# Performance work log

Hardware: AMD Instinct MI355X
Metric: run time of the kernel (lower is better)

The kernel has to match this reference:

```python
import jax, jax.numpy as jnp
import numpy as np
from jax import lax

K = 3
PAD = 1
STRIDE = 1


def setup_inputs() -> dict:
    key = jax.random.key(0)
    k1, k2, k3 = jax.random.split(key, 3)
    B, Cin, Cout, H, W = 4, 64, 64, 128, 128
    x = jax.random.normal(k1, (B, Cin, H, W), dtype=jnp.float32)
    # offset-generating conv weight: [2*K*K, Cin, K, K]
    w_offset = jax.random.normal(k2, (2 * K * K, Cin, K, K), dtype=jnp.float32) * 0.05
    # deformable conv weight: [Cout, Cin, K, K]
    w_deform = jax.random.normal(k3, (Cout, Cin, K, K), dtype=jnp.float32) * 0.05
    return {"x": x, "w_offset": w_offset, "w_deform": w_deform}


def _bilinear_sample_one(img, ys, xs):
    # img: [C, H, W]; ys, xs: [K2, Ho, Wo] float sampling coords
    H, W = img.shape[1], img.shape[2]
    y0 = jnp.floor(ys)
    x0 = jnp.floor(xs)
    wy = ys - y0  # frac weights, [K2, Ho, Wo]
    wx = xs - x0

    def gather(yi, xi):
        valid = (yi >= 0) & (yi <= H - 1) & (xi >= 0) & (xi <= W - 1)
        yc = jnp.clip(yi, 0, H - 1).astype(jnp.int32)
        xc = jnp.clip(xi, 0, W - 1).astype(jnp.int32)
        # img[:, yc, xc] -> [C, K2, Ho, Wo]; zero outside (torchvision zero-pad)
        return img[:, yc, xc] * valid[None].astype(img.dtype)

    v00 = gather(y0, x0)
    v01 = gather(y0, x0 + 1)
    v10 = gather(y0 + 1, x0)
    v11 = gather(y0 + 1, x0 + 1)
    w00 = ((1 - wy) * (1 - wx))[None]
    w01 = ((1 - wy) * wx)[None]
    w10 = (wy * (1 - wx))[None]
    w11 = (wy * wx)[None]
    return v00 * w00 + v01 * w01 + v10 * w10 + v11 * w11  # [C, K2, Ho, Wo]


def reference(x, w_offset, w_deform):
    B, Cin, H, W = x.shape
    Cout = w_deform.shape[0]
    K2 = K * K
    # 1) plain conv to produce offsets: [B, 2*K2, H, W]
    offset = lax.conv_general_dilated(
        x, w_offset, window_strides=(STRIDE, STRIDE),
        padding=((PAD, PAD), (PAD, PAD)),
        dimension_numbers=("NCHW", "OIHW", "NCHW"))
    Ho, Wo = offset.shape[2], offset.shape[3]
    # torchvision ordering: channel 2*k = dy, 2*k+1 = dx, taps row-major
    off = offset.reshape(B, K2, 2, Ho, Wo)
    dy, dx = off[:, :, 0], off[:, :, 1]  # [B, K2, Ho, Wo]
    # 2) base sampling grid per kernel tap
    kk = jnp.arange(K2)
    ki = (kk // K).astype(jnp.float32)  # tap row
    kj = (kk % K).astype(jnp.float32)   # tap col
    base_y = (jnp.arange(Ho, dtype=jnp.float32) * STRIDE - PAD)[None, :] + ki[:, None]  # [K2, Ho]
    base_x = (jnp.arange(Wo, dtype=jnp.float32) * STRIDE - PAD)[None, :] + kj[:, None]  # [K2, Wo]
    ys = base_y[None, :, :, None] + dy  # [B, K2, Ho, Wo]
    xs = base_x[None, :, None, :] + dx
    # 3) deformable bilinear gather: [B, Cin, K2, Ho, Wo]
    sampled = jax.vmap(_bilinear_sample_one)(x, ys, xs)
    # 4) weighted accumulation (the conv contraction)
    out = jnp.einsum("ock,bckhw->bohw", w_deform.reshape(Cout, Cin, K2), sampled)
    return out
```

## Files before the change

### kernel.cpp

```cpp
#include <hip/hip_runtime.h>


#define BATCH 4
#define CIN   64
#define COUT  64
#define HH    128
#define WW    128
#define HWPIX (HH*WW)

typedef __attribute__((ext_vector_type(8))) short short8;
typedef __attribute__((ext_vector_type(4))) float floatx4;
typedef __attribute__((ext_vector_type(2))) float f32x2;

__device__ __forceinline__ unsigned short f2bf(float f) {
  unsigned int u = __float_as_uint(f);
  unsigned int r = u + 0x7fffu + ((u >> 16) & 1u);
  return (unsigned short)(r >> 16);
}
__device__ __forceinline__ float bf2f(unsigned short h) { return __uint_as_float(((unsigned int)h) << 16); }
__device__ __forceinline__ float lo16f(unsigned int u) { return __uint_as_float(u << 16); }
__device__ __forceinline__ float hi16f(unsigned int u) { return __uint_as_float(u & 0xffff0000u); }

__device__ __forceinline__ unsigned int bilin2v(unsigned int u00, unsigned int u01,
                                                unsigned int u10, unsigned int u11,
                                                f32x2 w00, f32x2 w01, f32x2 w10, f32x2 w11) {
  f32x2 c00 = {lo16f(u00), hi16f(u00)};
  f32x2 c01 = {lo16f(u01), hi16f(u01)};
  f32x2 c10 = {lo16f(u10), hi16f(u10)};
  f32x2 c11 = {lo16f(u11), hi16f(u11)};
  f32x2 a = c00 * w00 + c01 * w01 + c10 * w10 + c11 * w11;
  unsigned int r;
  asm("v_cvt_pk_bf16_f32 %0, %1, %2" : "=v"(r) : "v"(a.x), "v"(a.y));
  return r;
}

__device__ __forceinline__ int swz(int a) { return a ^ (((a >> 9) & 3) << 4); }

__global__ __launch_bounds__(256) void pre_kernel(const float* __restrict__ x,
                                                  const float* __restrict__ wo,
                                                  const float* __restrict__ wd,
                                                  unsigned short* __restrict__ xThi,
                                                  unsigned short* __restrict__ xTlo,
                                                  unsigned short* __restrict__ wdA,
                                                  unsigned short* __restrict__ woAhi,
                                                  unsigned short* __restrict__ woAlo) {
  int tid = threadIdx.x;
  if (blockIdx.x < 4096) {
    __shared__ float tile[32][33];
    int t = blockIdx.x;
    int b = t >> 10, rem = t & 1023;
    int c0 = (rem >> 9) * 32, p0 = (rem & 511) * 32;
    int tx = tid & 31, ty = tid >> 5;
    const float* xb = x + (size_t)b * CIN * HWPIX;
    size_t boff = (size_t)b * HWPIX * CIN;
#pragma unroll
    for (int i = 0; i < 4; i++)
      tile[ty + i * 8][tx] = xb[(size_t)(c0 + ty + i * 8) * HWPIX + p0 + tx];
    __syncthreads();
#pragma unroll
    for (int i = 0; i < 2; i++) {
      int tt = tid + i * 256;
      int row = tt >> 4;
      int cp = tt & 15;
      float v0 = tile[cp * 2][row], v1 = tile[cp * 2 + 1][row];
      unsigned short h0 = f2bf(v0), h1 = f2bf(v1);
      unsigned short l0 = f2bf(v0 - bf2f(h0)), l1 = f2bf(v1 - bf2f(h1));
      size_t o = boff + (size_t)(p0 + row) * CIN + c0 + cp * 2;
      *(ushort2*)&xThi[o] = make_ushort2(h0, h1);
      *(ushort2*)&xTlo[o] = make_ushort2(l0, l1);
    }
  } else {
    int t = (blockIdx.x - 4096) * 256 + tid;
    if (t < 36864) {
      int j = t & 7, lane = (t >> 3) & 63, ct = (t >> 9) & 3, kc = (t >> 11) & 1, kk = t >> 12;
      int cout = ct * 16 + (lane & 15);
      int cin  = kc * 32 + (lane >> 4) * 8 + j;
      wdA[t] = f2bf(wd[(size_t)(cout * CIN + cin) * 9 + kk]);
    }
    int t2 = t - 36864;
    if (t2 >= 0 && t2 < 18432) {
      int j = t2 & 7, lane = (t2 >> 3) & 63, ct = (t2 >> 9) & 1, kc = (t2 >> 10) & 1, kk = t2 >> 11;
      int cout = ct * 16 + (lane & 15);
      int cin  = kc * 32 + (lane >> 4) * 8 + j;
      float v = (cout < 18) ? wo[(size_t)(cout * CIN + cin) * 9 + kk] : 0.f;
      unsigned short h = f2bf(v);
      woAhi[t2] = h;
      woAlo[t2] = f2bf(v - bf2f(h));
    }
  }
}

__global__ __launch_bounds__(256, 4) void fused_dcn_kernel(const unsigned short* __restrict__ xThi,
                                                           const unsigned short* __restrict__ xTlo,
                                                           const unsigned short* __restrict__ woAhi,
                                                           const unsigned short* __restrict__ woAlo,
                                                           const unsigned short* __restrict__ wdA,
                                                           float* __restrict__ out) {
  __shared__ unsigned short sBhi2[2][4096];
  __shared__ unsigned short sBlo2[2][4096];
  __shared__ float offL[18 * 64];
  char* sHc = (char*)sBhi2;
  char* sLc = (char*)sBlo2;

  int tid = threadIdx.x;
  int hw = blockIdx.x;
  int bid = (hw & 7) * 128 + (hw >> 3);
  int b = bid >> 8, r = bid & 255, y = r >> 1, x0 = (r & 1) << 6;

  int p1 = tid >> 2, si = tid & 3;
  int lane = tid & 63, w = tid >> 6;

  const unsigned short* xhib = xThi + (size_t)b * HWPIX * CIN;
  const unsigned short* xlob = xTlo + (size_t)b * HWPIX * CIN;

  int wq = p1 >> 4, iq = p1 & 15;
  int kcd = si >> 1, qb = si & 1;
  int wb0 = ((((wq * 2 + kcd) * 64) + qb * 32 + iq) * 8) * 2;
  int wb1 = wb0 + 256;
  int swb0 = swz(wb0), swb1 = swz(wb1);
  int brb0[4], brb1[4];
#pragma unroll
  for (int pg = 0; pg < 4; pg++) {
    brb0[pg] = swz(pg * 2048 + lane * 16);
    brb1[pg] = swz(pg * 2048 + 1024 + lane * 16);
  }

  int xp = x0 + p1;

  floatx4 oacc[2];
  oacc[0] = (floatx4){0.f, 0.f, 0.f, 0.f};
  oacc[1] = (floatx4){0.f, 0.f, 0.f, 0.f};
  int ctA = w & 1, pgA = (w >> 1) * 2;

  auto ldA = [&](int kk, uint4& h0, uint4& h1, uint4& l0, uint4& l1) {
    int ys = y - 1 + kk / 3;
    int xs = xp - 1 + kk % 3;
    bool valid = (ys >= 0) && (ys < HH) && (xs >= 0) && (xs < WW);
    h0 = (uint4){0, 0, 0, 0}; h1 = h0; l0 = h0; l1 = h0;
    if (valid) {
      const unsigned short* ph = xhib + (size_t)(ys * WW + xs) * CIN + si * 16;
      const unsigned short* pl = xlob + (size_t)(ys * WW + xs) * CIN + si * 16;
      h0 = *(const uint4*)ph; h1 = *(const uint4*)(ph + 8);
      l0 = *(const uint4*)pl; l1 = *(const uint4*)(pl + 8);
    }
  };
  auto stageA = [&](int nxt, const uint4& h0, const uint4& h1, const uint4& l0, const uint4& l1) {
    *(uint4*)(sHc + nxt * 8192 + swb0) = h0;
    *(uint4*)(sHc + nxt * 8192 + swb1) = h1;
    *(uint4*)(sLc + nxt * 8192 + swb0) = l0;
    *(uint4*)(sLc + nxt * 8192 + swb1) = l1;
  };
  auto mfmaA = [&](int kk, int cur) {
    const short8* Ah = (const short8*)(woAhi + (size_t)kk * 2048);
    const short8* Al = (const short8*)(woAlo + (size_t)kk * 2048);
    short8 ah0 = Ah[ctA * 64 + lane], ah1 = Ah[128 + ctA * 64 + lane];
    short8 al0 = Al[ctA * 64 + lane], al1 = Al[128 + ctA * 64 + lane];
#pragma unroll
    for (int pgi = 0; pgi < 2; pgi++) {
      int pg = pgA + pgi;
      short8 bh0 = *(const short8*)(sHc + cur * 8192 + brb0[pg]);
      short8 bh1 = *(const short8*)(sHc + cur * 8192 + brb1[pg]);
      short8 bl0 = *(const short8*)(sLc + cur * 8192 + brb0[pg]);
      short8 bl1 = *(const short8*)(sLc + cur * 8192 + brb1[pg]);
      oacc[pgi] = __builtin_amdgcn_mfma_f32_16x16x32_bf16(ah0, bh0, oacc[pgi], 0, 0, 0);
      oacc[pgi] = __builtin_amdgcn_mfma_f32_16x16x32_bf16(ah0, bl0, oacc[pgi], 0, 0, 0);
      oacc[pgi] = __builtin_amdgcn_mfma_f32_16x16x32_bf16(al0, bh0, oacc[pgi], 0, 0, 0);
      oacc[pgi] = __builtin_amdgcn_mfma_f32_16x16x32_bf16(ah1, bh1, oacc[pgi], 0, 0, 0);
      oacc[pgi] = __builtin_amdgcn_mfma_f32_16x16x32_bf16(ah1, bl1, oacc[pgi], 0, 0, 0);
      oacc[pgi] = __builtin_amdgcn_mfma_f32_16x16x32_bf16(al1, bh1, oacc[pgi], 0, 0, 0);
    }
  };

  {
    uint4 h0s[2], h1s[2], l0s[2], l1s[2];
    ldA(0, h0s[0], h1s[0], l0s[0], l1s[0]);
    stageA(0, h0s[0], h1s[0], l0s[0], l1s[0]);
    ldA(1, h0s[1], h1s[1], l0s[1], l1s[1]);
    __syncthreads();
#pragma unroll
    for (int kk = 0; kk < 9; kk++) {
      if (kk < 7) ldA(kk + 2, h0s[kk & 1], h1s[kk & 1], l0s[kk & 1], l1s[kk & 1]);
      __builtin_amdgcn_sched_barrier(0);
      if (kk < 8) stageA((kk + 1) & 1, h0s[(kk + 1) & 1], h1s[(kk + 1) & 1],
                         l0s[(kk + 1) & 1], l1s[(kk + 1) & 1]);
      mfmaA(kk, kk & 1);
      __syncthreads();
    }
  }

  {
    int rowb = (lane >> 4) * 4;
    int colb = pgA * 16 + (lane & 15);
#pragma unroll
    for (int pgi = 0; pgi < 2; pgi++)
#pragma unroll
      for (int rr = 0; rr < 4; rr++) {
        int row = ctA * 16 + rowb + rr;
        if (row < 18) offL[row * 64 + colb + pgi * 16] = oacc[pgi][rr];
      }
  }
  __syncthreads();

  floatx4 acc[4];
#pragma unroll
  for (int pg = 0; pg < 4; pg++) acc[pg] = (floatx4){0.f, 0.f, 0.f, 0.f};

  struct BS {
    float w00, w01, w10, w11;
    uint4 a00, a01, a10, a11, b00, b01, b10, b11;
  };
  auto ldB = [&](int kk) -> BS {
    BS s;
    float dy = offL[(2 * kk) * 64 + p1];
    float dx = offL[(2 * kk + 1) * 64 + p1];
    float ys = (float)(y - 1 + kk / 3) + dy;
    float xs = (float)(xp - 1 + kk % 3) + dx;
    float y0f = floorf(ys), x0f = floorf(xs);
    float wy = ys - y0f, wx = xs - x0f;
    int iy0 = (int)y0f, ix0 = (int)x0f;
    int iy1 = iy0 + 1, ix1 = ix0 + 1;
    s.w00 = (1.f - wy) * (1.f - wx); s.w01 = (1.f - wy) * wx;
    s.w10 = wy * (1.f - wx);         s.w11 = wy * wx;
    bool vy0 = (iy0 >= 0) && (iy0 < HH), vy1 = (iy1 >= 0) && (iy1 < HH);
    bool vx0 = (ix0 >= 0) && (ix0 < WW), vx1 = (ix1 >= 0) && (ix1 < WW);
    if (!(vy0 && vx0)) s.w00 = 0.f;
    if (!(vy0 && vx1)) s.w01 = 0.f;
    if (!(vy1 && vx0)) s.w10 = 0.f;
    if (!(vy1 && vx1)) s.w11 = 0.f;
    int cy0 = min(max(iy0, 0), HH - 1), cy1 = min(max(iy1, 0), HH - 1);
    int cx0 = min(max(ix0, 0), WW - 1), cx1 = min(max(ix1, 0), WW - 1);
    const unsigned short* q00 = xhib + (size_t)(cy0 * WW + cx0) * CIN + si * 16;
    const unsigned short* q01 = xhib + (size_t)(cy0 * WW + cx1) * CIN + si * 16;
    const unsigned short* q10 = xhib + (size_t)(cy1 * WW + cx0) * CIN + si * 16;
    const unsigned short* q11 = xhib + (size_t)(cy1 * WW + cx1) * CIN + si * 16;
    s.a00 = *(const uint4*)q00; s.a01 = *(const uint4*)q01;
    s.a10 = *(const uint4*)q10; s.a11 = *(const uint4*)q11;
    s.b00 = *(const uint4*)(q00 + 8); s.b01 = *(const uint4*)(q01 + 8);
    s.b10 = *(const uint4*)(q10 + 8); s.b11 = *(const uint4*)(q11 + 8);
    return s;
  };
  auto blendStoreB = [&](int nxt, const BS& s) {
    f32x2 w00 = {s.w00, s.w00}, w01 = {s.w01, s.w01};
    f32x2 w10 = {s.w10, s.w10}, w11 = {s.w11, s.w11};
    uint4 o0, o1;
    o0.x = bilin2v(s.a00.x, s.a01.x, s.a10.x, s.a11.x, w00, w01, w10, w11);
    o0.y = bilin2v(s.a00.y, s.a01.y, s.a10.y, s.a11.y, w00, w01, w10, w11);
    o0.z = bilin2v(s.a00.z, s.a01.z, s.a10.z, s.a11.z, w00, w01, w10, w11);
    o0.w = bilin2v(s.a00.w, s.a01.w, s.a10.w, s.a11.w, w00, w01, w10, w11);
    o1.x = bilin2v(s.b00.x, s.b01.x, s.b10.x, s.b11.x, w00, w01, w10, w11);
    o1.y = bilin2v(s.b00.y, s.b01.y, s.b10.y, s.b11.y, w00, w01, w10, w11);
    o1.z = bilin2v(s.b00.z, s.b01.z, s.b10.z, s.b11.z, w00, w01, w10, w11);
    o1.w = bilin2v(s.b00.w, s.b01.w, s.b10.w, s.b11.w, w00, w01, w10, w11);
    *(uint4*)(sHc + nxt * 8192 + swb0) = o0;
    *(uint4*)(sHc + nxt * 8192 + swb1) = o1;
  };
  auto mfmaB = [&](int kk, int cur) {
    const short8* Ap = (const short8*)(wdA + (size_t)kk * 4096);
    short8 a0 = Ap[w * 64 + lane];
    short8 a1 = Ap[256 + w * 64 + lane];
#pragma unroll
    for (int pg = 0; pg < 4; pg++) {
      short8 bv0 = *(const short8*)(sHc + cur * 8192 + brb0[pg]);
      short8 bv1 = *(const short8*)(sHc + cur * 8192 + brb1[pg]);
      acc[pg] = __builtin_amdgcn_mfma_f32_16x16x32_bf16(a0, bv0, acc[pg], 0, 0, 0);
      acc[pg] = __builtin_amdgcn_mfma_f32_16x16x32_bf16(a1, bv1, acc[pg], 0, 0, 0);
    }
  };

  {
    BS sb[2];
    sb[0] = ldB(0);
    blendStoreB(0, sb[0]);
    sb[1] = ldB(1);
    __syncthreads();
#pragma unroll
    for (int kk = 0; kk < 9; kk++) {
      if (kk < 7) sb[kk & 1] = ldB(kk + 2);
      __builtin_amdgcn_sched_barrier(0);
      if (kk < 8) blendStoreB((kk + 1) & 1, sb[(kk + 1) & 1]);
      mfmaB(kk, kk & 1);
      __syncthreads();
    }
  }

  int rowb = (lane >> 4) * 4;
  float* outb = out + (size_t)b * COUT * HWPIX + y * WW + x0 + (lane & 15);
#pragma unroll
  for (int pg = 0; pg < 4; pg++)
#pragma unroll
    for (int rr = 0; rr < 4; rr++)
      outb[(size_t)(w * 16 + rowb + rr) * HWPIX + pg * 16] = acc[pg][rr];
}

extern "C" void kernel_launch(void* const* d_in, const int* in_sizes, int n_in,
                              void* d_out, int out_size, void* d_ws, size_t ws_size,
                              hipStream_t stream) {
  const float* x  = (const float*)d_in[0];
  const float* wo = (const float*)d_in[1];
  const float* wd = (const float*)d_in[2];
  float* out = (float*)d_out;

  char* wsb = (char*)d_ws;
  unsigned short* xThi  = (unsigned short*)wsb;
  unsigned short* xTlo  = (unsigned short*)(wsb + 8388608);
  unsigned short* wdA   = (unsigned short*)(wsb + 16777216);
  unsigned short* woAhi = (unsigned short*)(wsb + 16777216 + 73728);
  unsigned short* woAlo = (unsigned short*)(wsb + 16850944 + 36864);

  pre_kernel<<<dim3(4096 + 216), dim3(256), 0, stream>>>(x, wo, wd, xThi, xTlo, wdA, woAhi, woAlo);
  fused_dcn_kernel<<<dim3(BATCH * HWPIX / 64), dim3(256), 0, stream>>>(xThi, xTlo, woAhi, woAlo, wdA, out);
}
```

Before: 104.9 us.

## Pad transposed input with zero halo and stream offset-conv tiles via global_load_lds

The preprocessing kernel now writes the bf16 hi/lo channel-last input into a 130x130 zero-padded buffer and zeroes the halo with extra blocks. The offset-conv stage drops per-thread bounds checks and register staging, and loads tiles straight into LDS with async global_load_lds using a new XOR swizzle for the MFMA B reads. The aim is to cut register pressure, VALU address work and the register-to-LDS copy in the first GEMM. The cost is a simpler single-stage prefetch pipeline and a slightly larger workspace.

```diff
diff --git a/kernel.cpp b/kernel.cpp
--- a/kernel.cpp
+++ b/kernel.cpp
@@ -7,6 +7,9 @@
 #define HH    128
 #define WW    128
 #define HWPIX (HH*WW)
+#define PADW  130
+#define PADROW (PADW*64)
+#define PADIMG (PADW*PADW*64)
 
 typedef __attribute__((ext_vector_type(8))) short short8;
 typedef __attribute__((ext_vector_type(4))) float floatx4;
@@ -36,11 +39,14 @@
 
 __device__ __forceinline__ int swz(int a) { return a ^ (((a >> 9) & 3) << 4); }
 
+typedef __attribute__((address_space(3))) void as3_void;
+typedef const __attribute__((address_space(1))) void as1_cvoid;
+
 __global__ __launch_bounds__(256) void pre_kernel(const float* __restrict__ x,
                                                   const float* __restrict__ wo,
                                                   const float* __restrict__ wd,
-                                                  unsigned short* __restrict__ xThi,
-                                                  unsigned short* __restrict__ xTlo,
+                                                  unsigned short* __restrict__ xThp,
+                                                  unsigned short* __restrict__ xTlp,
                                                   unsigned short* __restrict__ wdA,
                                                   unsigned short* __restrict__ woAhi,
                                                   unsigned short* __restrict__ woAlo) {
@@ -52,7 +58,8 @@
     int c0 = (rem >> 9) * 32, p0 = (rem & 511) * 32;
     int tx = tid & 31, ty = tid >> 5;
     const float* xb = x + (size_t)b * CIN * HWPIX;
-    size_t boff = (size_t)b * HWPIX * CIN;
+    size_t boff = (size_t)b * PADIMG;
+    int yy = p0 >> 7, xbase = p0 & 127;
 #pragma unroll
     for (int i = 0; i < 4; i++)
       tile[ty + i * 8][tx] = xb[(size_t)(c0 + ty + i * 8) * HWPIX + p0 + tx];
@@ -65,11 +72,11 @@
       float v0 = tile[cp * 2][row], v1 = tile[cp * 2 + 1][row];
       unsigned short h0 = f2bf(v0), h1 = f2bf(v1);
       unsigned short l0 = f2bf(v0 - bf2f(h0)), l1 = f2bf(v1 - bf2f(h1));
-      size_t o = boff + (size_t)(p0 + row) * CIN + c0 + cp * 2;
-      *(ushort2*)&xThi[o] = make_ushort2(h0, h1);
-      *(ushort2*)&xTlo[o] = make_ushort2(l0, l1);
-    }
-  } else {
+      size_t o = boff + (size_t)(yy + 1) * PADROW + (size_t)(xbase + row + 1) * 64 + c0 + cp * 2;
+      *(ushort2*)&xThp[o] = make_ushort2(h0, h1);
+      *(ushort2*)&xTlp[o] = make_ushort2(l0, l1);
+    }
+  } else if (blockIdx.x < 4312) {
     int t = (blockIdx.x - 4096) * 256 + tid;
     if (t < 36864) {
       int j = t & 7, lane = (t >> 3) & 63, ct = (t >> 9) & 3, kc = (t >> 11) & 1, kk = t >> 12;
@@ -87,11 +94,26 @@
       woAhi[t2] = h;
       woAlo[t2] = f2bf(v - bf2f(h));
     }
-  }
-}
-
-__global__ __launch_bounds__(256, 4) void fused_dcn_kernel(const unsigned short* __restrict__ xThi,
-                                                           const unsigned short* __restrict__ xTlo,
+  } else {
+    int iu = (blockIdx.x - 4312) * 256 + tid;
+    int sl = iu & 7;
+    int pu = iu >> 3;
+    int i = pu % 516;
+    int tmp = pu / 516;
+    int arr = tmp & 1, b = tmp >> 1;
+    int yp, xp;
+    if (i < 130)      { yp = 0;           xp = i; }
+    else if (i < 260) { yp = PADW - 1;    xp = i - 130; }
+    else if (i < 388) { yp = i - 260 + 1; xp = 0; }
+    else              { yp = i - 388 + 1; xp = PADW - 1; }
+    unsigned short* dst = (arr ? xTlp : xThp) + (size_t)b * PADIMG +
+                          (size_t)yp * PADROW + (size_t)xp * 64 + sl * 8;
+    *(uint4*)dst = (uint4){0, 0, 0, 0};
+  }
+}
+
+__global__ __launch_bounds__(256, 4) void fused_dcn_kernel(const unsigned short* __restrict__ xThp,
+                                                           const unsigned short* __restrict__ xTlp,
                                                            const unsigned short* __restrict__ woAhi,
                                                            const unsigned short* __restrict__ woAlo,
                                                            const unsigned short* __restrict__ wdA,
@@ -110,8 +132,25 @@
   int p1 = tid >> 2, si = tid & 3;
   int lane = tid & 63, w = tid >> 6;
 
-  const unsigned short* xhib = xThi + (size_t)b * HWPIX * CIN;
-  const unsigned short* xlob = xTlo + (size_t)b * HWPIX * CIN;
+  const unsigned short* xhp = xThp + (size_t)b * PADIMG;
+  const unsigned short* xlp = xTlp + (size_t)b * PADIMG;
+
+  int pxj[2], chj[2];
+#pragma unroll
+  for (int j = 0; j < 2; j++) {
+    int s = (w * 2 + j) * 64 + lane;
+    int u = s ^ ((s >> 3) & 7);
+    pxj[j] = u >> 3;
+    chj[j] = u & 7;
+  }
+  int rdA[4][2];
+#pragma unroll
+  for (int pg = 0; pg < 4; pg++)
+#pragma unroll
+    for (int kc = 0; kc < 2; kc++) {
+      int u = (pg * 16 + (lane & 15)) * 8 + kc * 4 + (lane >> 4);
+      rdA[pg][kc] = (u ^ (lane & 7)) * 16;
+    }
 
   int wq = p1 >> 4, iq = p1 & 15;
   int kcd = si >> 1, qb = si & 1;
@@ -132,23 +171,18 @@
   oacc[1] = (floatx4){0.f, 0.f, 0.f, 0.f};
   int ctA = w & 1, pgA = (w >> 1) * 2;
 
-  auto ldA = [&](int kk, uint4& h0, uint4& h1, uint4& l0, uint4& l1) {
-    int ys = y - 1 + kk / 3;
-    int xs = xp - 1 + kk % 3;
-    bool valid = (ys >= 0) && (ys < HH) && (xs >= 0) && (xs < WW);
-    h0 = (uint4){0, 0, 0, 0}; h1 = h0; l0 = h0; l1 = h0;
-    if (valid) {
-      const unsigned short* ph = xhib + (size_t)(ys * WW + xs) * CIN + si * 16;
-      const unsigned short* pl = xlob + (size_t)(ys * WW + xs) * CIN + si * 16;
-      h0 = *(const uint4*)ph; h1 = *(const uint4*)(ph + 8);
-      l0 = *(const uint4*)pl; l1 = *(const uint4*)(pl + 8);
-    }
-  };
-  auto stageA = [&](int nxt, const uint4& h0, const uint4& h1, const uint4& l0, const uint4& l1) {
-    *(uint4*)(sHc + nxt * 8192 + swb0) = h0;
-    *(uint4*)(sHc + nxt * 8192 + swb1) = h1;
-    *(uint4*)(sLc + nxt * 8192 + swb0) = l0;
-    *(uint4*)(sLc + nxt * 8192 + swb1) = l1;
+  auto issueA = [&](int kk, int bufsel) {
+    int kd = kk / 3, km = kk - kd * 3;
+    int rowbase = (y + kd) * PADROW + (x0 + km) * 64;
+#pragma unroll
+    for (int j = 0; j < 2; j++) {
+      const unsigned short* gh = xhp + rowbase + pxj[j] * 64 + chj[j] * 8;
+      const unsigned short* gl = xlp + rowbase + pxj[j] * 64 + chj[j] * 8;
+      __builtin_amdgcn_global_load_lds((as1_cvoid*)gh,
+          (as3_void*)(sHc + bufsel * 8192 + (w * 2 + j) * 1024), 16, 0, 0);
+      __builtin_amdgcn_global_load_lds((as1_cvoid*)gl,
+          (as3_void*)(sLc + bufsel * 8192 + (w * 2 + j) * 1024), 16, 0, 0);
+    }
   };
   auto mfmaA = [&](int kk, int cur) {
     const short8* Ah = (const short8*)(woAhi + (size_t)kk * 2048);
@@ -158,10 +192,10 @@
 #pragma unroll
     for (int pgi = 0; pgi < 2; pgi++) {
       int pg = pgA + pgi;
-      short8 bh0 = *(const short8*)(sHc + cur * 8192 + brb0[pg]);
-      short8 bh1 = *(const short8*)(sHc + cur * 8192 + brb1[pg]);
-      short8 bl0 = *(const short8*)(sLc + cur * 8192 + brb0[pg]);
-      short8 bl1 = *(const short8*)(sLc + cur * 8192 + brb1[pg]);
+      short8 bh0 = *(const short8*)(sHc + cur * 8192 + rdA[pg][0]);
+      short8 bh1 = *(const short8*)(sHc + cur * 8192 + rdA[pg][1]);
+      short8 bl0 = *(const short8*)(sLc + cur * 8192 + rdA[pg][0]);
+      short8 bl1 = *(const short8*)(sLc + cur * 8192 + rdA[pg][1]);
       oacc[pgi] = __builtin_amdgcn_mfma_f32_16x16x32_bf16(ah0, bh0, oacc[pgi], 0, 0, 0);
       oacc[pgi] = __builtin_amdgcn_mfma_f32_16x16x32_bf16(ah0, bl0, oacc[pgi], 0, 0, 0);
       oacc[pgi] = __builtin_amdgcn_mfma_f32_16x16x32_bf16(al0, bh0, oacc[pgi], 0, 0, 0);
@@ -171,21 +205,13 @@
     }
   };
 
-  {
-    uint4 h0s[2], h1s[2], l0s[2], l1s[2];
-    ldA(0, h0s[0], h1s[0], l0s[0], l1s[0]);
-    stageA(0, h0s[0], h1s[0], l0s[0], l1s[0]);
-    ldA(1, h0s[1], h1s[1], l0s[1], l1s[1]);
+  issueA(0, 0);
+  __syncthreads();
+#pragma unroll 1
+  for (int kk = 0; kk < 9; kk++) {
+    if (kk < 8) issueA(kk + 1, (kk + 1) & 1);
+    mfmaA(kk, kk & 1);
     __syncthreads();
-#pragma unroll
-    for (int kk = 0; kk < 9; kk++) {
-      if (kk < 7) ldA(kk + 2, h0s[kk & 1], h1s[kk & 1], l0s[kk & 1], l1s[kk & 1]);
-      __builtin_amdgcn_sched_barrier(0);
-      if (kk < 8) stageA((kk + 1) & 1, h0s[(kk + 1) & 1], h1s[(kk + 1) & 1],
-                         l0s[(kk + 1) & 1], l1s[(kk + 1) & 1]);
-      mfmaA(kk, kk & 1);
-      __syncthreads();
-    }
   }
 
   {
@@ -229,10 +255,10 @@
     if (!(vy1 && vx1)) s.w11 = 0.f;
     int cy0 = min(max(iy0, 0), HH - 1), cy1 = min(max(iy1, 0), HH - 1);
     int cx0 = min(max(ix0, 0), WW - 1), cx1 = min(max(ix1, 0), WW - 1);
-    const unsigned short* q00 = xhib + (size_t)(cy0 * WW + cx0) * CIN + si * 16;
-    const unsigned short* q01 = xhib + (size_t)(cy0 * WW + cx1) * CIN + si * 16;
-    const unsigned short* q10 = xhib + (size_t)(cy1 * WW + cx0) * CIN + si * 16;
-    const unsigned short* q11 = xhib + (size_t)(cy1 * WW + cx1) * CIN + si * 16;
+    const unsigned short* q00 = xhp + (size_t)(cy0 + 1) * PADROW + (size_t)(cx0 + 1) * 64 + si * 16;
+    const unsigned short* q01 = xhp + (size_t)(cy0 + 1) * PADROW + (size_t)(cx1 + 1) * 64 + si * 16;
+    const unsigned short* q10 = xhp + (size_t)(cy1 + 1) * PADROW + (size_t)(cx0 + 1) * 64 + si * 16;
+    const unsigned short* q11 = xhp + (size_t)(cy1 + 1) * PADROW + (size_t)(cx1 + 1) * 64 + si * 16;
     s.a00 = *(const uint4*)q00; s.a01 = *(const uint4*)q01;
     s.a10 = *(const uint4*)q10; s.a11 = *(const uint4*)q11;
     s.b00 = *(const uint4*)(q00 + 8); s.b01 = *(const uint4*)(q01 + 8);
@@ -301,12 +327,12 @@
   float* out = (float*)d_out;
 
   char* wsb = (char*)d_ws;
-  unsigned short* xThi  = (unsigned short*)wsb;
-  unsigned short* xTlo  = (unsigned short*)(wsb + 8388608);
-  unsigned short* wdA   = (unsigned short*)(wsb + 16777216);
-  unsigned short* woAhi = (unsigned short*)(wsb + 16777216 + 73728);
-  unsigned short* woAlo = (unsigned short*)(wsb + 16850944 + 36864);
-
-  pre_kernel<<<dim3(4096 + 216), dim3(256), 0, stream>>>(x, wo, wd, xThi, xTlo, wdA, woAhi, woAlo);
-  fused_dcn_kernel<<<dim3(BATCH * HWPIX / 64), dim3(256), 0, stream>>>(xThi, xTlo, woAhi, woAlo, wdA, out);
-}
+  unsigned short* xThp  = (unsigned short*)wsb;
+  unsigned short* xTlp  = (unsigned short*)(wsb + 8652800);
+  unsigned short* wdA   = (unsigned short*)(wsb + 17305600);
+  unsigned short* woAhi = (unsigned short*)(wsb + 17305600 + 73728);
+  unsigned short* woAlo = (unsigned short*)(wsb + 17379328 + 36864);
+
+  pre_kernel<<<dim3(4096 + 216 + 129), dim3(256), 0, stream>>>(x, wo, wd, xThp, xTlp, wdA, woAhi, woAlo);
+  fused_dcn_kernel<<<dim3(BATCH * HWPIX / 64), dim3(256), 0, stream>>>(xThp, xTlp, woAhi, woAlo, wdA, out);
+}
```

After: 106.7 us. No clear change (+1.7%).
